# Optimization experiments

Hardware: AMD Instinct MI355X
Metric: run time of the kernel (lower is better)

The kernel has to match this reference:

```python
import jax, jax.numpy as jnp
import numpy as np

N = 100000   # nodes
E = 1000000  # edges
G = 64       # graphs in batch
DIN, DH, DOUT = 128, 128, 64
BN_EPS = 1e-5


def setup_inputs() -> dict:
    key = jax.random.key(0)
    ks = jax.random.split(key, 20)
    inp = {}
    inp['x'] = jax.random.normal(ks[0], (N, DIN), dtype=jnp.float32)
    inp['edge_index'] = jax.random.randint(ks[1], (2, E), 0, N, dtype=jnp.int64)
    inp['batch'] = jnp.sort(jax.random.randint(ks[2], (N,), 0, G, dtype=jnp.int64))
    # GCN conv weights (stored [in, out]) + biases
    s = lambda k, i, o: jax.random.normal(k, (i, o), dtype=jnp.float32) / np.sqrt(i)
    inp['W1'] = s(ks[3], DIN, DH);  inp['b1'] = jnp.zeros((DH,), jnp.float32)
    inp['W2'] = s(ks[4], DH, DH);   inp['b2'] = jnp.zeros((DH,), jnp.float32)
    inp['W3'] = s(ks[5], DH, DOUT); inp['b3'] = jnp.zeros((DOUT,), jnp.float32)
    # BatchNorm params/buffers (eval mode)
    inp['g1'] = jnp.ones((DH,), jnp.float32);  inp['beta1'] = jnp.zeros((DH,), jnp.float32)
    inp['g2'] = jnp.ones((DH,), jnp.float32);  inp['beta2'] = jnp.zeros((DH,), jnp.float32)
    inp['mean1'] = jnp.zeros((DH,), jnp.float32); inp['var1'] = jnp.ones((DH,), jnp.float32)
    inp['mean2'] = jnp.zeros((DH,), jnp.float32); inp['var2'] = jnp.ones((DH,), jnp.float32)
    # GlobalAttention gate_nn: Linear(DOUT,DH) ReLU Linear(DH,1)
    inp['Wg1'] = s(ks[6], DOUT, DH); inp['bg1'] = jnp.zeros((DH,), jnp.float32)
    inp['Wg2'] = s(ks[7], DH, 1);    inp['bg2'] = jnp.zeros((1,), jnp.float32)
    # head MLP: Linear(DOUT,DH) ReLU Linear(DH,DOUT)
    inp['Wm1'] = s(ks[8], DOUT, DH); inp['bm1'] = jnp.zeros((DH,), jnp.float32)
    inp['Wm2'] = s(ks[9], DH, DOUT); inp['bm2'] = jnp.zeros((DOUT,), jnp.float32)
    return inp


def _gcn_conv(x, W, b, src, dst):
    # PyG GCNConv: add self-loops, sym-normalize, linear, scatter-sum, bias
    h = x @ W                                            # [N, out]
    deg = jnp.ones((N,), h.dtype).at[dst].add(1.0)       # in-degree + self-loop
    dinv = jax.lax.rsqrt(deg)
    norm = dinv[src] * dinv[dst]                         # [E]
    msg = h[src] * norm[:, None]                         # gather + scale
    out = jax.ops.segment_sum(msg, dst, num_segments=N)  # scatter
    out = out + h * (dinv * dinv)[:, None]               # self-loop term
    return out + b


def _bn(x, g, beta, mean, var):
    return (x - mean) * jax.lax.rsqrt(var + BN_EPS) * g + beta


def reference(x, edge_index, batch, W1, b1, W2, b2, W3, b3,
              g1, beta1, g2, beta2, mean1, var1, mean2, var2,
              Wg1, bg1, Wg2, bg2, Wm1, bm1, Wm2, bm2):
    src, dst = edge_index[0], edge_index[1]
    h = jax.nn.relu(_bn(_gcn_conv(x, W1, b1, src, dst), g1, beta1, mean1, var1))
    h = jax.nn.relu(_bn(_gcn_conv(h, W2, b2, src, dst), g2, beta2, mean2, var2))
    h = _gcn_conv(h, W3, b3, src, dst)                   # [N, DOUT]
    # GlobalAttention pooling: per-graph softmax of gate scores
    gate = jax.nn.relu(h @ Wg1 + bg1) @ Wg2 + bg2        # [N, 1]
    gate = gate[:, 0]
    m = jax.ops.segment_max(gate, batch, num_segments=G)
    e = jnp.exp(gate - m[batch])
    s = jax.ops.segment_sum(e, batch, num_segments=G)
    a = e / s[batch]                                     # [N]
    pooled = jax.ops.segment_sum(h * a[:, None], batch, num_segments=G)  # [G, DOUT]
    # MLP head (dropout off in eval)
    return jax.nn.relu(pooled @ Wm1 + bm1) @ Wm2 + bm2   # [G, DOUT]
```

## Files before the change

### kernel.cpp

```cpp
#include <hip/hip_runtime.h>
#include <hip/hip_bf16.h>
#include <hip/hip_fp16.h>
#include <math.h>

#define NN 100000
#define EE 1000000
#define GG 64
#define BN_EPS 1e-5f
#define CPB 16
#define EB 4096
#define NBLK ((EE + EB - 1) / EB)
#define NBUCK ((NN + 511) / 512)

typedef __attribute__((ext_vector_type(8))) short bf16x8;
typedef __attribute__((ext_vector_type(4))) float f32x4;

__device__ inline short f2bf(float f) {
  unsigned u = __float_as_uint(f);
  u = u + 0x7fff + ((u >> 16) & 1);
  return (short)(u >> 16);
}
__device__ inline float bf2f(short h) {
  return __uint_as_float(((unsigned)(unsigned short)h) << 16);
}

__device__ inline unsigned fenc(float f) {
  int b = __float_as_int(f);
  return (b < 0) ? ~(unsigned)b : ((unsigned)b | 0x80000000u);
}
__device__ inline float fdec(unsigned u) {
  int b = (u & 0x80000000u) ? (int)(u & 0x7fffffffu) : (int)~u;
  return __int_as_float(b);
}

__device__ inline void acc2(float& a0, float& a1, unsigned u) {
  asm("v_fma_mix_f32 %0, %2, 1.0, %0 op_sel:[0,0,0] op_sel_hi:[1,0,0]\n\t"
      "v_fma_mix_f32 %1, %2, 1.0, %1 op_sel:[1,0,0] op_sel_hi:[1,0,0]"
      : "+v"(a0), "+v"(a1)
      : "v"(u));
}
__device__ inline void acc8(float* a, uint4 u) {
  acc2(a[0], a[1], u.x);
  acc2(a[2], a[3], u.y);
  acc2(a[4], a[5], u.z);
  acc2(a[6], a[7], u.w);
}
__device__ inline uint4 zsel(uint4 u, int ok) {
  uint4 r;
  r.x = ok ? u.x : 0u;
  r.y = ok ? u.y : 0u;
  r.z = ok ? u.z : 0u;
  r.w = ok ? u.w : 0u;
  return r;
}

__global__ __launch_bounds__(256) void k_bhist(const int* __restrict__ dst,
                                               int* __restrict__ bhist, int E) {
  __shared__ int h[256];
  int t = threadIdx.x;
  h[t] = 0;
  __syncthreads();
  int base = blockIdx.x * EB;
#pragma unroll
  for (int j = 0; j < EB / 256; ++j) {
    int i = base + j * 256 + t;
    if (i < E) atomicAdd(&h[dst[i] >> 9], 1);
  }
  __syncthreads();
  bhist[blockIdx.x * 256 + t] = h[t];
}

__global__ __launch_bounds__(256) void k_bscan1(int* __restrict__ bhist,
                                                int* __restrict__ btot) {
  __shared__ int s[256];
  int bin = blockIdx.x, t = threadIdx.x;
  int v = (t < NBLK) ? bhist[t * 256 + bin] : 0;
  s[t] = v;
  __syncthreads();
  for (int o = 1; o < 256; o <<= 1) {
    int u = (t >= o) ? s[t - o] : 0;
    __syncthreads();
    s[t] += u;
    __syncthreads();
  }
  if (t < NBLK) bhist[t * 256 + bin] = s[t] - v;
  if (t == 255) btot[bin] = s[255];
}

__global__ __launch_bounds__(256) void k_bscan2(const int* __restrict__ btot,
                                                int* __restrict__ bstart) {
  __shared__ int s[256];
  int t = threadIdx.x;
  int v = btot[t];
  s[t] = v;
  __syncthreads();
  for (int o = 1; o < 256; o <<= 1) {
    int u = (t >= o) ? s[t - o] : 0;
    __syncthreads();
    s[t] += u;
    __syncthreads();
  }
  bstart[t] = s[t] - v;
}

__global__ __launch_bounds__(256) void k_bscat(const int* __restrict__ src,
                                               const int* __restrict__ dst,
                                               const int* __restrict__ bhist,
                                               const int* __restrict__ bstart,
                                               int2* __restrict__ pairs, int E) {
  __shared__ int h[256];
  __shared__ int base[256];
  int t = threadIdx.x;
  h[t] = 0;
  __syncthreads();
  int b0 = blockIdx.x * EB;
  int ds[EB / 256], rk[EB / 256];
#pragma unroll
  for (int j = 0; j < EB / 256; ++j) {
    int i = b0 + j * 256 + t;
    if (i < E) {
      int d = dst[i];
      ds[j] = d;
      rk[j] = atomicAdd(&h[d >> 9], 1);
    } else
      ds[j] = -1;
  }
  __syncthreads();
  base[t] = bstart[t] + bhist[blockIdx.x * 256 + t];
  __syncthreads();
#pragma unroll
  for (int j = 0; j < EB / 256; ++j) {
    int i = b0 + j * 256 + t;
    if (ds[j] >= 0) {
      int pos = base[ds[j] >> 9] + rk[j];
      pairs[pos] = make_int2(src[i], ds[j]);
    }
  }
}

__global__ __launch_bounds__(256) void k_bfill(const int2* __restrict__ pairs,
                                               const int* __restrict__ bstart,
                                               int* __restrict__ rowstart,
                                               int* __restrict__ eidx,
                                               float* __restrict__ dinv, int N,
                                               int E) {
  __shared__ int h[512];
  __shared__ int ex[512];
  __shared__ int ps[256];
  const int b = blockIdx.x;
  const int n0 = b << 9;
  const int e0 = bstart[b], e1 = bstart[b + 1];
  const int t = threadIdx.x;
  h[t] = 0;
  h[t + 256] = 0;
  __syncthreads();
  for (int i = e0 + t; i < e1; i += 256) atomicAdd(&h[pairs[i].y - n0], 1);
  __syncthreads();
  int v0 = h[2 * t], v1 = h[2 * t + 1];
  int sp = v0 + v1;
  ps[t] = sp;
  __syncthreads();
  for (int o = 1; o < 256; o <<= 1) {
    int u = (t >= o) ? ps[t - o] : 0;
    __syncthreads();
    ps[t] += u;
    __syncthreads();
  }
  int ex0 = ps[t] - sp;
  ex[2 * t] = ex0;
  ex[2 * t + 1] = ex0 + v0;
  __syncthreads();
  for (int i = t; i < 512; i += 256) {
    int node = n0 + i;
    if (node < N) {
      rowstart[node] = e0 + ex[i];
      dinv[node] = rsqrtf(1.0f + (float)h[i]);
    }
  }
  if (b == 0 && t == 0) rowstart[N] = E;
  __syncthreads();
  for (int i = e0 + t; i < e1; i += 256) {
    int2 p = pairs[i];
    int r = atomicAdd(&ex[p.y - n0], 1);
    eidx[e0 + r] = p.x;
  }
}

__global__ __launch_bounds__(256) void k_wsplit(const float* __restrict__ W1,
                                                const float* __restrict__ W2,
                                                const float* __restrict__ W3,
                                                const float* __restrict__ Wg1,
                                                short* __restrict__ wt) {
  int i = blockIdx.x * 256 + threadIdx.x;
  const float* W;
  short *hi, *lo;
  int K, M, idx;
  if (i < 16384) {
    W = W1; hi = wt; lo = wt + 16384; K = 128; M = 128; idx = i;
  } else if (i < 32768) {
    W = W2; hi = wt + 32768; lo = wt + 49152; K = 128; M = 128; idx = i - 16384;
  } else if (i < 40960) {
    W = W3; hi = wt + 65536; lo = wt + 73728; K = 128; M = 64; idx = i - 32768;
  } else {
    W = Wg1; hi = wt + 81920; lo = wt + 90112; K = 64; M = 128; idx = i - 40960;
  }
  int k = idx / M, n = idx % M;
  float w = W[idx];
  short h = f2bf(w);
  hi[n * K + k] = h;
  lo[n * K + k] = f2bf(w - bf2f(h));
}

__global__ __launch_bounds__(256) void k_bnprep(
    const float* __restrict__ g1, const float* __restrict__ b1,
    const float* __restrict__ m1, const float* __restrict__ v1,
    const float* __restrict__ g2, const float* __restrict__ b2,
    const float* __restrict__ m2, const float* __restrict__ v2,
    float* __restrict__ s1, float* __restrict__ h1, float* __restrict__ s2,
    float* __restrict__ h2) {
  int i = threadIdx.x;
  if (i < 128) {
    float s = g1[i] * rsqrtf(v1[i] + BN_EPS);
    s1[i] = s;
    h1[i] = b1[i] - m1[i] * s;
  } else {
    int j = i - 128;
    float s = g2[j] * rsqrtf(v2[j] + BN_EPS);
    s2[j] = s;
    h2[j] = b2[j] - m2[j] * s;
  }
}

template <int K, int M, int CTB, int AIN, int DINV, int GATE, int OUTH>
__device__ __forceinline__ void mgemm_body(
    short* lds, const float* __restrict__ Xf, const short* __restrict__ Xhi,
    const short* __restrict__ Xlo, const short* __restrict__ Wthi,
    const short* __restrict__ Wtlo, const float* __restrict__ dinv,
    const float* __restrict__ gbias, const float* __restrict__ Wg2v,
    const float* __restrict__ bg2v, void* __restrict__ Y,
    float* __restrict__ gate, int nrows) {
  constexpr int NC = K / 32;
  constexpr int KP = K + 8;
  constexpr int R = 2;
  const int lane = threadIdx.x & 63;
  const int wave = threadIdx.x >> 6;
  const int m16 = lane & 15;
  const int quad = lane >> 4;
  const int rowbase = blockIdx.x * 128 + wave * 32;
  const int cbase = blockIdx.y * CTB * 16;

  bf16x8 ahi[R][NC], alo[R][NC];
#pragma unroll
  for (int t = 0; t < R; ++t) {
    const int arow = rowbase + t * 16 + m16;
    const bool rok = arow < nrows;
#pragma unroll
    for (int c = 0; c < NC; ++c) {
      const int k0 = c * 32 + quad * 8;
      if constexpr (AIN) {
        if (rok) {
          ahi[t][c] = *(const bf16x8*)(Xhi + (size_t)arow * K + k0);
          alo[t][c] = *(const bf16x8*)(Xlo + (size_t)arow * K + k0);
        } else {
          ahi[t][c] = bf16x8{0, 0, 0, 0, 0, 0, 0, 0};
          alo[t][c] = bf16x8{0, 0, 0, 0, 0, 0, 0, 0};
        }
      } else {
        float4 v0 = make_float4(0.f, 0.f, 0.f, 0.f), v1 = v0;
        if (rok) {
          v0 = *(const float4*)(Xf + (size_t)arow * K + k0);
          v1 = *(const float4*)(Xf + (size_t)arow * K + k0 + 4);
        }
        float vv[8] = {v0.x, v0.y, v0.z, v0.w, v1.x, v1.y, v1.z, v1.w};
#pragma unroll
        for (int j = 0; j < 8; ++j) {
          short h = f2bf(vv[j]);
          ahi[t][c][j] = h;
          alo[t][c][j] = f2bf(vv[j] - bf2f(h));
        }
      }
    }
  }

  {
    constexpr int ELEMS = CTB * 16 * K;
#pragma unroll
    for (int i = threadIdx.x * 8; i < ELEMS; i += 256 * 8) {
      const int r = i / K, c = i % K;
      *(bf16x8*)(&lds[r * KP + c]) =
          *(const bf16x8*)(Wthi + (size_t)(cbase + r) * K + c);
      *(bf16x8*)(&lds[CTB * 16 * KP + r * KP + c]) =
          *(const bf16x8*)(Wtlo + (size_t)(cbase + r) * K + c);
    }
  }

  float dv[R][4];
  if constexpr (DINV && !GATE) {
#pragma unroll
    for (int t = 0; t < R; ++t)
#pragma unroll
      for (int r = 0; r < 4; ++r) {
        int row = rowbase + t * 16 + quad * 4 + r;
        dv[t][r] = (row < nrows) ? dinv[row] : 0.f;
      }
  }

  float gp[R][4];
  if constexpr (GATE) {
#pragma unroll
    for (int t = 0; t < R; ++t)
#pragma unroll
      for (int r = 0; r < 4; ++r) gp[t][r] = 0.f;
  }

  __syncthreads();

  f32x4 accs[CTB][R];
#pragma unroll
  for (int ct = 0; ct < CTB; ++ct) {
    bf16x8 bhi[NC], blo[NC];
    const int wrow = (ct * 16 + m16) * KP + quad * 8;
#pragma unroll
    for (int c = 0; c < NC; ++c) {
      bhi[c] = *(const bf16x8*)(&lds[wrow + c * 32]);
      blo[c] = *(const bf16x8*)(&lds[CTB * 16 * KP + wrow + c * 32]);
    }
#pragma unroll
    for (int t = 0; t < R; ++t) {
      f32x4 acc = {0.f, 0.f, 0.f, 0.f};
#pragma unroll
      for (int c = 0; c < NC; ++c) {
        acc = __builtin_amdgcn_mfma_f32_16x16x32_bf16(ahi[t][c], bhi[c], acc, 0, 0, 0);
        acc = __builtin_amdgcn_mfma_f32_16x16x32_bf16(ahi[t][c], blo[c], acc, 0, 0, 0);
        acc = __builtin_amdgcn_mfma_f32_16x16x32_bf16(alo[t][c], bhi[c], acc, 0, 0, 0);
      }
      if constexpr (GATE) {
        const int col = cbase + ct * 16 + m16;
        const float gb = gbias[col], wg = Wg2v[col];
#pragma unroll
        for (int r = 0; r < 4; ++r) gp[t][r] += fmaxf(acc[r] + gb, 0.f) * wg;
      } else {
        accs[ct][t] = acc;
      }
    }
  }

  if constexpr (GATE) {
#pragma unroll
    for (int o = 1; o < 16; o <<= 1) {
#pragma unroll
      for (int t = 0; t < R; ++t)
#pragma unroll
        for (int r = 0; r < 4; ++r) gp[t][r] += __shfl_xor(gp[t][r], o, 64);
    }
    if (m16 == 0) {
      const float b2 = bg2v[0];
#pragma unroll
      for (int t = 0; t < R; ++t)
#pragma unroll
        for (int r = 0; r < 4; ++r) {
          const int row = rowbase + t * 16 + quad * 4 + r;
          if (row < nrows) gate[row] = gp[t][r] + b2;
        }
    }
  } else {
    constexpr int COLS = CTB * 16;
    constexpr int SP = COLS + 8;
    __syncthreads();
#pragma unroll
    for (int ct = 0; ct < CTB; ++ct)
#pragma unroll
      for (int t = 0; t < R; ++t)
#pragma unroll
        for (int r = 0; r < 4; ++r) {
          const int row_l = wave * 32 + t * 16 + quad * 4 + r;
          float v = accs[ct][t][r];
          if constexpr (DINV) v *= dv[t][r];
          __half hv = __float2half(v);
          lds[row_l * SP + ct * 16 + m16] = *(short*)&hv;
        }
    __syncthreads();
    constexpr int TOT = 128 * COLS;
#pragma unroll
    for (int p = 0; p < TOT / (256 * 8); ++p) {
      const int idx8 = (p * 256 + threadIdx.x) * 8;
      const int row_l = idx8 / COLS;
      const int col0 = idx8 % COLS;
      const int grow = blockIdx.x * 128 + row_l;
      if (grow < nrows) {
        bf16x8 v = *(const bf16x8*)(&lds[row_l * SP + col0]);
        *(bf16x8*)((__half*)Y + (size_t)grow * M + cbase + col0) = v;
      }
    }
  }
}

#define MGEMM_ARGS                                                            \
  const float *Xf, const short *Xhi, const short *Xlo, const short *Wthi,     \
      const short *Wtlo, const float *dinv, const float *gbias,               \
      const float *Wg2v, const float *bg2v, void *Y, float *gate, int nrows

#define DEF_MGEMM(NAME, K, M, CTB, AIN, DINV, GATE, OUTH)                     \
  __global__ __launch_bounds__(256, 3) void NAME(MGEMM_ARGS) {                \
    __shared__ short lds[2 * CTB * 16 * (K + 8)];                             \
    mgemm_body<K, M, CTB, AIN, DINV, GATE, OUTH>(lds, Xf, Xhi, Xlo, Wthi,     \
                                                 Wtlo, dinv, gbias, Wg2v,     \
                                                 bg2v, Y, gate, nrows);       \
  }

DEF_MGEMM(k_mgemm1, 128, 128, 4, 0, 1, 0, 1)
DEF_MGEMM(k_mgemm2, 128, 128, 4, 1, 1, 0, 1)
DEF_MGEMM(k_mgemm3, 128, 64, 4, 1, 1, 0, 1)
DEF_MGEMM(k_mgemmg, 64, 128, 8, 0, 0, 1, 0)

template <int M, int EPI>
__device__ __forceinline__ void agg_body(
    const __half* __restrict__ hp, const int* __restrict__ rowstart,
    const int* __restrict__ eidx, const float* __restrict__ dinv,
    const float* __restrict__ bias, const float* __restrict__ bns,
    const float* __restrict__ bnh, float* __restrict__ outf,
    short* __restrict__ ohi, short* __restrict__ olo, int N) {
  constexpr int LPR = M / 8;
  constexpr int NPW = 64 / (2 * LPR);
  const int wv = (blockIdx.x * 256 + threadIdx.x) >> 6;
  const int lane = threadIdx.x & 63;
  const int grp = lane / (2 * LPR);
  const int slot = (lane / LPR) & 1;
  const int sub = lane % LPR;
  const int w = wv * NPW + grp;
  if (w >= N) return;
  const unsigned subo = (unsigned)sub * 16u;
  const float di = dinv[w];
  const int lo = rowstart[w], hi = rowstart[w + 1];
  const int hi1 = hi - 1;
  const char* hpb = (const char*)hp;
  float a[8] = {0.f, 0.f, 0.f, 0.f, 0.f, 0.f, 0.f, 0.f};

  int e = lo + slot;
  while (e < hi) {
    int idx[8], ss[8];
    uint4 uu[8];
#pragma unroll
    for (int p = 0; p < 8; ++p) {
      idx[p] = e + 2 * p;
      ss[p] = eidx[min(idx[p], hi1)];
    }
#pragma unroll
    for (int p = 0; p < 8; ++p)
      uu[p] = *(const uint4*)(hpb + ((unsigned)ss[p] * (unsigned)(M * 2) + subo));
#pragma unroll
    for (int p = 0; p < 8; ++p) {
      uu[p] = zsel(uu[p], idx[p] < hi);
      acc8(a, uu[p]);
    }
    e += 16;
  }
#pragma unroll
  for (int j = 0; j < 8; ++j) a[j] += __shfl_xor(a[j], LPR, 64);

  if (slot != 0) return;
  uint4 us = *(const uint4*)(hpb + ((unsigned)w * (unsigned)(M * 2) + subo));
  acc8(a, us);
  float4 b0 = *(const float4*)(bias + sub * 8);
  float4 b1 = *(const float4*)(bias + sub * 8 + 4);
  float r[8];
  r[0] = a[0] * di + b0.x;
  r[1] = a[1] * di + b0.y;
  r[2] = a[2] * di + b0.z;
  r[3] = a[3] * di + b0.w;
  r[4] = a[4] * di + b1.x;
  r[5] = a[5] * di + b1.y;
  r[6] = a[6] * di + b1.z;
  r[7] = a[7] * di + b1.w;
  if constexpr (EPI) {
    float4 s0 = *(const float4*)(bns + sub * 8);
    float4 s1 = *(const float4*)(bns + sub * 8 + 4);
    float4 h0 = *(const float4*)(bnh + sub * 8);
    float4 h1 = *(const float4*)(bnh + sub * 8 + 4);
    float sv[8] = {s0.x, s0.y, s0.z, s0.w, s1.x, s1.y, s1.z, s1.w};
    float hv[8] = {h0.x, h0.y, h0.z, h0.w, h1.x, h1.y, h1.z, h1.w};
    short hs[8], ls[8];
#pragma unroll
    for (int j = 0; j < 8; ++j) {
      float ev = fmaxf(r[j] * sv[j] + hv[j], 0.f);
      short hb = f2bf(ev);
      float res = ev - bf2f(hb);
      hs[j] = hb;
      ls[j] = (short)(__float_as_uint(res) >> 16);
    }
    *(short4*)(ohi + (size_t)w * M + sub * 8) = make_short4(hs[0], hs[1], hs[2], hs[3]);
    *(short4*)(ohi + (size_t)w * M + sub * 8 + 4) = make_short4(hs[4], hs[5], hs[6], hs[7]);
    *(short4*)(olo + (size_t)w * M + sub * 8) = make_short4(ls[0], ls[1], ls[2], ls[3]);
    *(short4*)(olo + (size_t)w * M + sub * 8 + 4) = make_short4(ls[4], ls[5], ls[6], ls[7]);
  } else {
    *(float4*)(outf + (size_t)w * M + sub * 8) = make_float4(r[0], r[1], r[2], r[3]);
    *(float4*)(outf + (size_t)w * M + sub * 8 + 4) = make_float4(r[4], r[5], r[6], r[7]);
  }
}

#define AGG_ARGS                                                              \
  const __half *hp, const int *rowstart, const int *eidx, const float *dinv,  \
      const float *bias, const float *bns, const float *bnh, float *outf,     \
      short *ohi, short *olo, int N

#define DEF_AGG(NAME, M, EPI)                                                 \
  __global__ __launch_bounds__(256) void NAME(AGG_ARGS) {                     \
    agg_body<M, EPI>(hp, rowstart, eidx, dinv, bias, bns, bnh, outf, ohi,     \
                     olo, N);                                                 \
  }

DEF_AGG(k_agg1, 128, 1)
DEF_AGG(k_agg2, 128, 1)
DEF_AGG(k_agg3, 64, 0)

__global__ __launch_bounds__(128) void k_gbounds(const int* __restrict__ batch,
                                                 int* __restrict__ gstart,
                                                 int N) {
  int g = threadIdx.x;
  if (g > GG) return;
  int lo = 0, hi = N;
  while (lo < hi) {
    int mid = (lo + hi) >> 1;
    if (batch[mid] < g) lo = mid + 1;
    else hi = mid;
  }
  gstart[g] = lo;
}

__global__ __launch_bounds__(256) void k_pmax(const float* __restrict__ gate,
                                              const int* __restrict__ gstart,
                                              unsigned* __restrict__ gmaxu) {
  __shared__ unsigned red[256];
  const int g = blockIdx.x / CPB;
  const int c = blockIdx.x % CPB;
  const int lo = gstart[g], hi = gstart[g + 1];
  const int len = hi - lo;
  const int b0 = lo + (int)(((long long)len * c) / CPB);
  const int b1 = lo + (int)(((long long)len * (c + 1)) / CPB);
  unsigned mx = 0u;
  for (int i = b0 + threadIdx.x; i < b1; i += 256) mx = max(mx, fenc(gate[i]));
  red[threadIdx.x] = mx;
  __syncthreads();
  for (int o = 128; o; o >>= 1) {
    if (threadIdx.x < o)
      red[threadIdx.x] = max(red[threadIdx.x], red[threadIdx.x + o]);
    __syncthreads();
  }
  if (threadIdx.x == 0 && red[0] != 0u) atomicMax(&gmaxu[g], red[0]);
}

__global__ __launch_bounds__(256) void k_psum(const float* __restrict__ gate,
                                              const float* __restrict__ h3,
                                              const unsigned* __restrict__ gmaxu,
                                              const int* __restrict__ gstart,
                                              float* __restrict__ pooledw,
                                              float* __restrict__ ssum) {
  __shared__ float accs[4][64];
  __shared__ float ses[4];
  const int g = blockIdx.x / CPB;
  const int c = blockIdx.x % CPB;
  const int lo = gstart[g], hi = gstart[g + 1];
  const int len = hi - lo;
  const int b0 = lo + (int)(((long long)len * c) / CPB);
  const int b1 = lo + (int)(((long long)len * (c + 1)) / CPB);
  const int wave = threadIdx.x >> 6, lane = threadIdx.x & 63;
  const float m = fdec(gmaxu[g]);
  float acc = 0.f, se = 0.f;
  for (int i = b0 + wave; i < b1; i += 4) {
    float e = expf(gate[i] - m);
    acc += e * h3[(size_t)i * 64 + lane];
    se += e;
  }
  accs[wave][lane] = acc;
  if (lane == 0) ses[wave] = se;
  __syncthreads();
  if (threadIdx.x < 64) {
    float a = accs[0][threadIdx.x] + accs[1][threadIdx.x] +
              accs[2][threadIdx.x] + accs[3][threadIdx.x];
    if (a != 0.f) atomicAdd(&pooledw[g * 64 + threadIdx.x], a);
  }
  if (threadIdx.x == 64) {
    float s = ses[0] + ses[1] + ses[2] + ses[3];
    if (s != 0.f) atomicAdd(&ssum[g], s);
  }
}

__global__ __launch_bounds__(256) void k_head(const float* __restrict__ pooledw,
                                              const float* __restrict__ ssum,
                                              const float* __restrict__ Wm1,
                                              const float* __restrict__ bm1,
                                              const float* __restrict__ Wm2,
                                              const float* __restrict__ bm2,
                                              float* __restrict__ out) {
  __shared__ float P[64 * 64];
  __shared__ float T[64 * 128];
  int tid = threadIdx.x;
  for (int i = tid; i < 4096; i += 256) {
    float s = ssum[i >> 6];
    P[i] = pooledw[i] * ((s > 0.f) ? 1.0f / s : 0.f);
  }
  __syncthreads();
  for (int e = tid; e < 8192; e += 256) {
    int r = e >> 7, c = e & 127;
    float a = bm1[c];
    for (int k = 0; k < 64; ++k) a += P[r * 64 + k] * Wm1[k * 128 + c];
    T[e] = fmaxf(a, 0.f);
  }
  __syncthreads();
  for (int e = tid; e < 4096; e += 256) {
    int r = e >> 6, c = e & 63;
    float a = bm2[c];
    for (int k = 0; k < 128; ++k) a += T[r * 128 + k] * Wm2[k * 64 + c];
    out[e] = a;
  }
}

extern "C" void kernel_launch(void* const* d_in, const int* in_sizes, int n_in,
                              void* d_out, int out_size, void* d_ws,
                              size_t ws_size, hipStream_t stream) {
  const int N = NN, E = EE;
  const float* x = (const float*)d_in[0];
  const int* ei = (const int*)d_in[1];
  const int* batch = (const int*)d_in[2];
  const float* W1 = (const float*)d_in[3];
  const float* b1 = (const float*)d_in[4];
  const float* W2 = (const float*)d_in[5];
  const float* b2 = (const float*)d_in[6];
  const float* W3 = (const float*)d_in[7];
  const float* b3 = (const float*)d_in[8];
  const float* g1 = (const float*)d_in[9];
  const float* beta1 = (const float*)d_in[10];
  const float* g2 = (const float*)d_in[11];
  const float* beta2 = (const float*)d_in[12];
  const float* mean1 = (const float*)d_in[13];
  const float* var1 = (const float*)d_in[14];
  const float* mean2 = (const float*)d_in[15];
  const float* var2 = (const float*)d_in[16];
  const float* Wg1 = (const float*)d_in[17];
  const float* bg1 = (const float*)d_in[18];
  const float* Wg2 = (const float*)d_in[19];
  const float* bg2 = (const float*)d_in[20];
  const float* Wm1 = (const float*)d_in[21];
  const float* bm1 = (const float*)d_in[22];
  const float* Wm2 = (const float*)d_in[23];
  const float* bm2 = (const float*)d_in[24];
  float* out = (float*)d_out;

  const int* src = ei;
  const int* dst = ei + E;

  char* wsb = (char*)d_ws;
  size_t off = 0;
  auto alloc = [&](size_t elems) -> void* {
    void* p = wsb + off;
    off += elems * 4;
    return p;
  };
  int* rowstart = (int*)alloc(N + 4);
  int* eidx = (int*)alloc(E);
  int2* pairs = (int2*)alloc((size_t)E * 2);
  int* bhist = (int*)alloc(NBLK * 256 + 256);
  int* btot = (int*)alloc(256);
  int* bstart = (int*)alloc(256);
  float* dinv = (float*)alloc(N);
  float* gate = (float*)alloc(N);
  __half* hbuf = (__half*)alloc((size_t)N * 64);
  short* ahi_p = (short*)alloc((size_t)N * 64);
  short* alo_p = (short*)alloc((size_t)N * 64);
  float* fbuf = (float*)alloc((size_t)N * 64);
  short* wt = (short*)alloc(49152);
  float* bn1s = (float*)alloc(128);
  float* bn1h = (float*)alloc(128);
  float* bn2s = (float*)alloc(128);
  float* bn2h = (float*)alloc(128);
  float* pooledw = (float*)alloc(GG * 64);
  float* ssum = (float*)alloc(GG);
  unsigned* gmaxu = (unsigned*)alloc(GG);
  int* gstart = (int*)alloc(GG + 4);
  (void)ws_size;
  (void)n_in;
  (void)in_sizes;
  (void)out_size;

  hipMemsetAsync(pooledw, 0, (GG * 64 + GG + GG) * sizeof(float), stream);
  k_bhist<<<NBLK, 256, 0, stream>>>(dst, bhist, E);
  k_bscan1<<<256, 256, 0, stream>>>(bhist, btot);
  k_bscan2<<<1, 256, 0, stream>>>(btot, bstart);
  k_bscat<<<NBLK, 256, 0, stream>>>(src, dst, bhist, bstart, pairs, E);
  k_bfill<<<NBUCK, 256, 0, stream>>>(pairs, bstart, rowstart, eidx, dinv, N, E);

  k_wsplit<<<192, 256, 0, stream>>>(W1, W2, W3, Wg1, wt);
  k_bnprep<<<1, 256, 0, stream>>>(g1, beta1, mean1, var1, g2, beta2, mean2,
                                  var2, bn1s, bn1h, bn2s, bn2h);
  k_gbounds<<<1, 128, 0, stream>>>(batch, gstart, N);

  const int gbb = (N + 127) / 128;
  const int ab128 = (N + 7) / 8;
  const int ab64 = (N + 15) / 16;

  k_mgemm1<<<dim3(gbb, 2), 256, 0, stream>>>(
      x, nullptr, nullptr, wt, wt + 16384, dinv, nullptr, nullptr, nullptr,
      hbuf, nullptr, N);
  k_agg1<<<ab128, 256, 0, stream>>>(hbuf, rowstart, eidx, dinv, b1, bn1s,
                                    bn1h, nullptr, ahi_p, alo_p, N);

  k_mgemm2<<<dim3(gbb, 2), 256, 0, stream>>>(
      nullptr, ahi_p, alo_p, wt + 32768, wt + 49152, dinv, nullptr, nullptr,
      nullptr, hbuf, nullptr, N);
  k_agg2<<<ab128, 256, 0, stream>>>(hbuf, rowstart, eidx, dinv, b2, bn2s,
                                    bn2h, nullptr, ahi_p, alo_p, N);

  k_mgemm3<<<dim3(gbb, 1), 256, 0, stream>>>(
      nullptr, ahi_p, alo_p, wt + 65536, wt + 73728, dinv, nullptr, nullptr,
      nullptr, hbuf, nullptr, N);
  k_agg3<<<ab64, 256, 0, stream>>>(hbuf, rowstart, eidx, dinv, b3, nullptr,
                                   nullptr, fbuf, nullptr, nullptr, N);

  k_mgemmg<<<dim3(gbb, 1), 256, 0, stream>>>(
      fbuf, nullptr, nullptr, wt + 81920, wt + 90112, nullptr, bg1, Wg2, bg2,
      nullptr, gate, N);

  k_pmax<<<GG * CPB, 256, 0, stream>>>(gate, gstart, gmaxu);
  k_psum<<<GG * CPB, 256, 0, stream>>>(gate, fbuf, gmaxu, gstart, pooledw,
                                       ssum);

  k_head<<<1, 256, 0, stream>>>(pooledw, ssum, Wm1, bm1, Wm2, bm2, out);
}
```

Before: 462.8 us.

## Merge prep kernels into one launch and halve GEMM column tiles per block

Folds the weight split, BatchNorm prep, graph-boundary search and the pooled-buffer memset into one k_prep launch, cutting three launches and a memset from the stream. Separately, the three GCN GEMMs now cover half as many column tiles per block, launch twice as many column blocks, and raise the occupancy hint from 3 to 4 blocks per unit. This trades more parallelism and occupancy against repeated loading of the A-row tiles across the extra column blocks.

```diff
diff --git a/kernel.cpp b/kernel.cpp
--- a/kernel.cpp
+++ b/kernel.cpp
@@ -186,48 +186,59 @@
   }
 }
 
-__global__ __launch_bounds__(256) void k_wsplit(const float* __restrict__ W1,
-                                                const float* __restrict__ W2,
-                                                const float* __restrict__ W3,
-                                                const float* __restrict__ Wg1,
-                                                short* __restrict__ wt) {
-  int i = blockIdx.x * 256 + threadIdx.x;
-  const float* W;
-  short *hi, *lo;
-  int K, M, idx;
-  if (i < 16384) {
-    W = W1; hi = wt; lo = wt + 16384; K = 128; M = 128; idx = i;
-  } else if (i < 32768) {
-    W = W2; hi = wt + 32768; lo = wt + 49152; K = 128; M = 128; idx = i - 16384;
-  } else if (i < 40960) {
-    W = W3; hi = wt + 65536; lo = wt + 73728; K = 128; M = 64; idx = i - 32768;
+__global__ __launch_bounds__(256) void k_prep(
+    const float* __restrict__ W1, const float* __restrict__ W2,
+    const float* __restrict__ W3, const float* __restrict__ Wg1,
+    short* __restrict__ wt, const float* __restrict__ g1,
+    const float* __restrict__ b1, const float* __restrict__ m1,
+    const float* __restrict__ v1, const float* __restrict__ g2,
+    const float* __restrict__ b2, const float* __restrict__ m2,
+    const float* __restrict__ v2, float* __restrict__ s1,
+    float* __restrict__ h1, float* __restrict__ s2, float* __restrict__ h2,
+    const int* __restrict__ batch, int* __restrict__ gstart,
+    float* __restrict__ pooledw, int N) {
+  const int b = blockIdx.x, t = threadIdx.x;
+  if (b < 192) {
+    int i = b * 256 + t;
+    const float* W;
+    short *hi, *lo;
+    int K, M, idx;
+    if (i < 16384) {
+      W = W1; hi = wt; lo = wt + 16384; K = 128; M = 128; idx = i;
+    } else if (i < 32768) {
+      W = W2; hi = wt + 32768; lo = wt + 49152; K = 128; M = 128; idx = i - 16384;
+    } else if (i < 40960) {
+      W = W3; hi = wt + 65536; lo = wt + 73728; K = 128; M = 64; idx = i - 32768;
+    } else {
+      W = Wg1; hi = wt + 81920; lo = wt + 90112; K = 64; M = 128; idx = i - 40960;
+    }
+    int k = idx / M, n = idx % M;
+    float w = W[idx];
+    short h = f2bf(w);
+    hi[n * K + k] = h;
+    lo[n * K + k] = f2bf(w - bf2f(h));
+  } else if (b == 192) {
+    if (t < 128) {
+      float s = g1[t] * rsqrtf(v1[t] + BN_EPS);
+      s1[t] = s;
+      h1[t] = b1[t] - m1[t] * s;
+    } else {
+      int j = t - 128;
+      float s = g2[j] * rsqrtf(v2[j] + BN_EPS);
+      s2[j] = s;
+      h2[j] = b2[j] - m2[j] * s;
+    }
   } else {
-    W = Wg1; hi = wt + 81920; lo = wt + 90112; K = 64; M = 128; idx = i - 40960;
-  }
-  int k = idx / M, n = idx % M;
-  float w = W[idx];
-  short h = f2bf(w);
-  hi[n * K + k] = h;
-  lo[n * K + k] = f2bf(w - bf2f(h));
-}
-
-__global__ __launch_bounds__(256) void k_bnprep(
-    const float* __restrict__ g1, const float* __restrict__ b1,
-    const float* __restrict__ m1, const float* __restrict__ v1,
-    const float* __restrict__ g2, const float* __restrict__ b2,
-    const float* __restrict__ m2, const float* __restrict__ v2,
-    float* __restrict__ s1, float* __restrict__ h1, float* __restrict__ s2,
-    float* __restrict__ h2) {
-  int i = threadIdx.x;
-  if (i < 128) {
-    float s = g1[i] * rsqrtf(v1[i] + BN_EPS);
-    s1[i] = s;
-    h1[i] = b1[i] - m1[i] * s;
-  } else {
-    int j = i - 128;
-    float s = g2[j] * rsqrtf(v2[j] + BN_EPS);
-    s2[j] = s;
-    h2[j] = b2[j] - m2[j] * s;
+    if (t <= GG) {
+      int lo = 0, hi = N;
+      while (lo < hi) {
+        int mid = (lo + hi) >> 1;
+        if (batch[mid] < t) lo = mid + 1;
+        else hi = mid;
+      }
+      gstart[t] = lo;
+    }
+    for (int i = t; i < GG * 64 + GG + GG; i += 256) pooledw[i] = 0.f;
   }
 }
 
@@ -400,18 +411,18 @@
       const short *Wtlo, const float *dinv, const float *gbias,               \
       const float *Wg2v, const float *bg2v, void *Y, float *gate, int nrows
 
-#define DEF_MGEMM(NAME, K, M, CTB, AIN, DINV, GATE, OUTH)                     \
-  __global__ __launch_bounds__(256, 3) void NAME(MGEMM_ARGS) {                \
+#define DEF_MGEMM(NAME, K, M, CTB, AIN, DINV, GATE, OUTH, WPE)                \
+  __global__ __launch_bounds__(256, WPE) void NAME(MGEMM_ARGS) {              \
     __shared__ short lds[2 * CTB * 16 * (K + 8)];                             \
     mgemm_body<K, M, CTB, AIN, DINV, GATE, OUTH>(lds, Xf, Xhi, Xlo, Wthi,     \
                                                  Wtlo, dinv, gbias, Wg2v,     \
                                                  bg2v, Y, gate, nrows);       \
   }
 
-DEF_MGEMM(k_mgemm1, 128, 128, 4, 0, 1, 0, 1)
-DEF_MGEMM(k_mgemm2, 128, 128, 4, 1, 1, 0, 1)
-DEF_MGEMM(k_mgemm3, 128, 64, 4, 1, 1, 0, 1)
-DEF_MGEMM(k_mgemmg, 64, 128, 8, 0, 0, 1, 0)
+DEF_MGEMM(k_mgemm1, 128, 128, 2, 0, 1, 0, 1, 4)
+DEF_MGEMM(k_mgemm2, 128, 128, 2, 1, 1, 0, 1, 4)
+DEF_MGEMM(k_mgemm3, 128, 64, 2, 1, 1, 0, 1, 4)
+DEF_MGEMM(k_mgemmg, 64, 128, 8, 0, 0, 1, 0, 3)
 
 template <int M, int EPI>
 __device__ __forceinline__ void agg_body(
@@ -512,20 +523,6 @@
 DEF_AGG(k_agg1, 128, 1)
 DEF_AGG(k_agg2, 128, 1)
 DEF_AGG(k_agg3, 64, 0)
-
-__global__ __launch_bounds__(128) void k_gbounds(const int* __restrict__ batch,
-                                                 int* __restrict__ gstart,
-                                                 int N) {
-  int g = threadIdx.x;
-  if (g > GG) return;
-  int lo = 0, hi = N;
-  while (lo < hi) {
-    int mid = (lo + hi) >> 1;
-    if (batch[mid] < g) lo = mid + 1;
-    else hi = mid;
-  }
-  gstart[g] = lo;
-}
 
 __global__ __launch_bounds__(256) void k_pmax(const float* __restrict__ gate,
                                               const int* __restrict__ gstart,
@@ -682,35 +679,33 @@
   (void)in_sizes;
   (void)out_size;
 
-  hipMemsetAsync(pooledw, 0, (GG * 64 + GG + GG) * sizeof(float), stream);
   k_bhist<<<NBLK, 256, 0, stream>>>(dst, bhist, E);
   k_bscan1<<<256, 256, 0, stream>>>(bhist, btot);
   k_bscan2<<<1, 256, 0, stream>>>(btot, bstart);
   k_bscat<<<NBLK, 256, 0, stream>>>(src, dst, bhist, bstart, pairs, E);
   k_bfill<<<NBUCK, 256, 0, stream>>>(pairs, bstart, rowstart, eidx, dinv, N, E);
 
-  k_wsplit<<<192, 256, 0, stream>>>(W1, W2, W3, Wg1, wt);
-  k_bnprep<<<1, 256, 0, stream>>>(g1, beta1, mean1, var1, g2, beta2, mean2,
-                                  var2, bn1s, bn1h, bn2s, bn2h);
-  k_gbounds<<<1, 128, 0, stream>>>(batch, gstart, N);
+  k_prep<<<194, 256, 0, stream>>>(W1, W2, W3, Wg1, wt, g1, beta1, mean1, var1,
+                                  g2, beta2, mean2, var2, bn1s, bn1h, bn2s,
+                                  bn2h, batch, gstart, pooledw, N);
 
   const int gbb = (N + 127) / 128;
   const int ab128 = (N + 7) / 8;
   const int ab64 = (N + 15) / 16;
 
-  k_mgemm1<<<dim3(gbb, 2), 256, 0, stream>>>(
+  k_mgemm1<<<dim3(gbb, 4), 256, 0, stream>>>(
       x, nullptr, nullptr, wt, wt + 16384, dinv, nullptr, nullptr, nullptr,
       hbuf, nullptr, N);
   k_agg1<<<ab128, 256, 0, stream>>>(hbuf, rowstart, eidx, dinv, b1, bn1s,
                                     bn1h, nullptr, ahi_p, alo_p, N);
 
-  k_mgemm2<<<dim3(gbb, 2), 256, 0, stream>>>(
+  k_mgemm2<<<dim3(gbb, 4), 256, 0, stream>>>(
       nullptr, ahi_p, alo_p, wt + 32768, wt + 49152, dinv, nullptr, nullptr,
       nullptr, hbuf, nullptr, N);
   k_agg2<<<ab128, 256, 0, stream>>>(hbuf, rowstart, eidx, dinv, b2, bn2s,
                                     bn2h, nullptr, ahi_p, alo_p, N);
 
-  k_mgemm3<<<dim3(gbb, 1), 256, 0, stream>>>(
+  k_mgemm3<<<dim3(gbb, 2), 256, 0, stream>>>(
       nullptr, ahi_p, alo_p, wt + 65536, wt + 73728, dinv, nullptr, nullptr,
       nullptr, hbuf, nullptr, N);
   k_agg3<<<ab64, 256, 0, stream>>>(hbuf, rowstart, eidx, dinv, b3, nullptr,
```

Measured after the change: 509.8 us. 10.2% more time.
